# Performance work log

Hardware: AMD Instinct MI355X
Metric: run time of the kernel (lower is better)

The kernel has to match this reference:

```python
import jax, jax.numpy as jnp
import numpy as np

H_SZ, W_SZ = 24, 24  # size for location=2 (H*W == N3)

def _ln(x, g, b, eps=1e-5):
    m = jnp.mean(x, axis=-1, keepdims=True)
    v = jnp.var(x, axis=-1, keepdims=True)
    return (x - m) / jnp.sqrt(v + eps) * g + b

def _cross_attn(value, x2, Wp, bp):
    # key = softmax(x2^T, dim=1) == softmax over channels; query = softmax over tokens
    k = jax.nn.softmax(x2, axis=2)   # [B,M,C], softmax over C
    q = jax.nn.softmax(x2, axis=1)   # [B,M,C], softmax over M
    ctx = jnp.einsum('bnc,bmc->bnm', value, k)   # value @ key
    att = jnp.einsum('bnm,bmc->bnc', ctx, q)     # context @ query
    return att @ Wp.T + bp

def _dwconv(x, Wdw, bdw, Hh, Ww):
    B, N, C = x.shape
    t = x.transpose(0, 2, 1).reshape(B, C, Hh, Ww)
    y = jax.lax.conv_general_dilated(t, Wdw, (1, 1), 'SAME',
                                     feature_group_count=C,
                                     dimension_numbers=('NCHW', 'OIHW', 'NCHW'))
    y = y + bdw[None, :, None, None]
    return y.reshape(B, C, N).transpose(0, 2, 1)

def setup_inputs() -> dict:
    key = jax.random.key(0)
    ks = jax.random.split(key, 16)
    B = 4; d0, d1, d2 = 128, 256, 512
    N1, N2, N3 = 96 * 96, 48 * 48, 24 * 24
    s = 0.02
    dh = 4 * d2
    inp = {}
    inp['x']  = jax.random.normal(ks[0], (B, N1, d0), jnp.float32)
    inp['x2'] = jax.random.normal(ks[1], (B, N2, d1), jnp.float32)
    inp['x3'] = jax.random.normal(ks[2], (B, N3, d2), jnp.float32)
    inp['W_lin']  = jax.random.normal(ks[3], (d2, d0)) * s   # linear: d0->d2
    inp['W_lin2'] = jax.random.normal(ks[4], (d2, d1)) * s   # linear2: d1->d2
    inp['W_lin3'] = jax.random.normal(ks[5], (d1, d0)) * s   # linear3: d0->d1
    inp['W_lin4'] = jax.random.normal(ks[6], (d2, d1)) * s   # linear4: d1->d2
    inp['w'] = jnp.ones((1,), jnp.float32)
    inp['Wp1'] = jax.random.normal(ks[7], (d2, d2)) * s;  inp['bp1'] = jnp.zeros((d2,))
    inp['Wp2'] = jax.random.normal(ks[8], (d2, d2)) * s;  inp['bp2'] = jnp.zeros((d2,))
    inp['Wp3'] = jax.random.normal(ks[9], (d1, d1)) * s;  inp['bp3'] = jnp.zeros((d1,))
    inp['Wp4'] = jax.random.normal(ks[10], (d2, d2)) * s; inp['bp4'] = jnp.zeros((d2,))
    inp['g_norm'] = jnp.ones((d2,)); inp['b_norm'] = jnp.zeros((d2,))
    inp['Wfc1'] = jax.random.normal(ks[11], (dh, d2)) * s; inp['bfc1'] = jnp.zeros((dh,))
    inp['Wdw']  = jax.random.normal(ks[12], (dh, 1, 3, 3)) * s; inp['bdw'] = jnp.zeros((dh,))
    inp['g_ln1'] = jnp.ones((dh,)); inp['b_ln1'] = jnp.zeros((dh,))
    inp['Wfc2'] = jax.random.normal(ks[13], (d2, dh)) * s; inp['bfc2'] = jnp.zeros((d2,))
    return inp

def reference(x, x2, x3, W_lin, W_lin2, W_lin3, W_lin4, w,
              Wp1, bp1, Wp2, bp2, Wp3, bp3, Wp4, bp4,
              g_norm, b_norm, Wfc1, bfc1, Wdw, bdw, g_ln1, b_ln1, Wfc2, bfc2):
    # location == 2 branch
    image  = x  @ W_lin.T    # [B,N1,d2]
    image2 = x2 @ W_lin2.T   # [B,N2,d2]
    image4 = x  @ W_lin3.T   # [B,N1,d1]
    atten1 = _cross_attn(x3, image,  Wp1, bp1)
    atten2 = _cross_attn(x3, image2, Wp2, bp2)
    a3 = _cross_attn(x2, image4, Wp3, bp3)   # [B,N2,d1]
    a3 = a3 @ W_lin4.T                        # [B,N2,d2]
    atten3 = _cross_attn(x3, a3, Wp4, bp4)    # [B,N3,d2]
    f = jax.nn.sigmoid(w)
    other = (1.0 - f) / 2.0
    atten_ = f * atten3 + other * atten2 + other * atten1
    atten = x3 + atten_
    an = _ln(atten, g_norm, b_norm)
    # MixFFN_skip (fc1 computed once; torch computes it twice with same result)
    h = an @ Wfc1.T + bfc1
    dw = _dwconv(h, Wdw, bdw, H_SZ, W_SZ)
    ax = jax.nn.gelu(_ln(dw + h, g_ln1, b_ln1), approximate=False)
    out = ax @ Wfc2.T + bfc2
    return atten + out
```

## Files before the change

### kernel.cpp

```cpp
#include <hip/hip_runtime.h>
#include <hip/hip_bf16.h>
#include <math.h>

typedef long long i64;
typedef __attribute__((ext_vector_type(8))) short short8v;
typedef __attribute__((ext_vector_type(4))) short short4v;
typedef __attribute__((ext_vector_type(4))) float float4v;

#define SPITCH 72
#define NCV 16

__device__ __forceinline__ float ldv(const void* p, i64 idx, int isBf16) {
  return isBf16 ? __bfloat162float(((const __hip_bfloat16*)p)[idx])
                : ((const float*)p)[idx];
}
__device__ __forceinline__ unsigned short bf16bits(float f) {
  __hip_bfloat16 h = __float2bfloat16(f);
  return *(unsigned short*)&h;
}
__device__ __forceinline__ float bits2f(unsigned short u) {
  union { unsigned int ui; float fl; } cv; cv.ui = ((unsigned int)u) << 16;
  return cv.fl;
}

__global__ void detect_dtype(const unsigned short* w, int* dt) {
  dt[0] = (w[0] == 0) ? 0 : 1;
}

struct CvArgs {
  const void* src[NCV];
  unsigned short* dst[NCV];
  i64 n[NCV];
  int blkStart[NCV + 1];
};
__global__ __launch_bounds__(256) void convert_many(const int* dt, CvArgs a) {
  int au = dt[0];
  int bid = blockIdx.x;
  int lo = 0;
  #pragma unroll
  for (int i = 0; i < NCV; ++i) if (bid >= a.blkStart[i + 1]) lo = i + 1;
  const void* s = a.src[lo];
  unsigned short* d = a.dst[lo];
  i64 n = a.n[lo];
  i64 base = ((i64)(bid - a.blkStart[lo]) * 256 + threadIdx.x) * 4;
  if (base + 4 <= n) {
    if (au) {
      *(short4v*)&d[base] = *(const short4v*)&((const unsigned short*)s)[base];
    } else {
      float4v v = *(const float4v*)&((const float*)s)[base];
      short4v o;
      #pragma unroll
      for (int j = 0; j < 4; ++j) o[j] = (short)bf16bits(v[j]);
      *(short4v*)&d[base] = o;
    }
  } else {
    for (; base < n; ++base) d[base] = bf16bits(ldv(s, base, au));
  }
}

__global__ void transpose_dw(const int* dt, const void* Wdw, unsigned short* Wdwt) {
  int au = dt[0];
  int i = blockIdx.x * 256 + threadIdx.x;
  if (i >= 9 * 2048) return;
  int k = i / 2048, ch = i % 2048;
  Wdwt[i] = bf16bits(ldv(Wdw, (i64)ch * 9 + k, au));
}

__global__ __launch_bounds__(256) void gemm_mfma_bt(
    const int* dt,
    const unsigned short* A, i64 bsA,
    const unsigned short* Bt, i64 bsB,
    const void* bias, int biasDt,
    const void* add, int addDt, i64 bsAdd,
    void* C, i64 bsC, int outMode,
    int M, int N, int K, int flags,
    const void* wPtr, int alphaMode,
    float* csP, float* rsP)
{
  __shared__ unsigned short Ash[64 * SPITCH];
  __shared__ unsigned short Bsh[64 * SPITCH];
  __shared__ unsigned short LT[64 * SPITCH];

  const int au = dt[0];
  const int bDt = (biasDt == 2) ? au : biasDt;
  const int aDt = (addDt == 2) ? au : addDt;

  const int b  = blockIdx.z;
  const int m0 = blockIdx.y * 64;
  const int n0 = blockIdx.x * 64;
  const int t = threadIdx.x;
  const int lane = t & 63, wave = t >> 6;
  const int wr = (wave >> 1) * 32, wc = (wave & 1) * 32;
  const int quad = lane >> 4, l15 = lane & 15;
  const unsigned short* Ab = A + (i64)b * bsA;
  const unsigned short* Bb = Bt + (i64)b * bsB;
  const int sr = t >> 3, sg = (t & 7) * 8;

  float alpha = 1.0f;
  if (alphaMode) {
    float w0 = ldv(wPtr, 0, au);
    float f = 1.0f / (1.0f + expf(-w0));
    alpha = (alphaMode == 2) ? f : (1.0f - f) * 0.5f;
  }

  float4v acc00 = {0.f,0.f,0.f,0.f}, acc01 = {0.f,0.f,0.f,0.f};
  float4v acc10 = {0.f,0.f,0.f,0.f}, acc11 = {0.f,0.f,0.f,0.f};

  for (int k0 = 0; k0 < K; k0 += 64) {
    #pragma unroll
    for (int p = 0; p < 2; ++p) {
      int rr = sr + p * 32;
      *(short8v*)&Ash[rr * SPITCH + sg] = *(const short8v*)&Ab[(i64)(m0 + rr) * K + k0 + sg];
      *(short8v*)&Bsh[rr * SPITCH + sg] = *(const short8v*)&Bb[(i64)(n0 + rr) * K + k0 + sg];
    }
    __syncthreads();
    #pragma unroll
    for (int ks = 0; ks < 2; ++ks) {
      int ko = ks * 32 + quad * 8;
      short8v a0 = *(const short8v*)&Ash[(wr + l15) * SPITCH + ko];
      short8v a1 = *(const short8v*)&Ash[(wr + 16 + l15) * SPITCH + ko];
      short8v b0 = *(const short8v*)&Bsh[(wc + l15) * SPITCH + ko];
      short8v b1 = *(const short8v*)&Bsh[(wc + 16 + l15) * SPITCH + ko];
      acc00 = __builtin_amdgcn_mfma_f32_16x16x32_bf16(a0, b0, acc00, 0, 0, 0);
      acc01 = __builtin_amdgcn_mfma_f32_16x16x32_bf16(a0, b1, acc01, 0, 0, 0);
      acc10 = __builtin_amdgcn_mfma_f32_16x16x32_bf16(a1, b0, acc10, 0, 0, 0);
      acc11 = __builtin_amdgcn_mfma_f32_16x16x32_bf16(a1, b1, acc11, 0, 0, 0);
    }
    __syncthreads();
  }

  float* Cf = (float*)C;
  unsigned short* Ch = (unsigned short*)C;

  if (outMode == 2) {
    #pragma unroll
    for (int rg = 0; rg < 4; ++rg) {
      #pragma unroll
      for (int sub = 0; sub < 4; ++sub) {
        int lr = wr + quad * 4 + rg + (sub >> 1) * 16;
        int lc = wc + l15 + (sub & 1) * 16;
        float v = (sub == 0 ? acc00[rg] : sub == 1 ? acc01[rg] :
                   sub == 2 ? acc10[rg] : acc11[rg]) * alpha;
        if (bias) v += ldv(bias, n0 + lc, bDt);
        if (flags & 1) v = expf(v);
        LT[lc * SPITCH + lr] = bf16bits(v);
      }
    }
    __syncthreads();
    #pragma unroll
    for (int p = 0; p < 2; ++p) {
      int rr = sr + p * 32;
      short8v vv = *(short8v*)&LT[rr * SPITCH + sg];
      *(short8v*)(Ch + (i64)b * bsC + (i64)(n0 + rr) * M + m0 + sg) = vv;
    }
    if (csP) {
      if (t < 64) {
        const unsigned short* Lr = &LT[t * SPITCH];
        float s = 0.f;
        #pragma unroll
        for (int i = 0; i < 64; ++i) s += bits2f(Lr[i]);
        atomicAdd(&csP[(i64)b * N + n0 + t], s);
      } else if (t < 128) {
        int tok = t - 64;
        float s = 0.f;
        #pragma unroll
        for (int i = 0; i < 64; ++i) s += bits2f(LT[i * SPITCH + tok]);
        atomicAdd(&rsP[(i64)b * M + m0 + tok], s);
      }
    }
    return;
  }

  #pragma unroll
  for (int rg = 0; rg < 4; ++rg) {
    #pragma unroll
    for (int sub = 0; sub < 4; ++sub) {
      int lr = wr + quad * 4 + rg + (sub >> 1) * 16;
      int lc = wc + l15 + (sub & 1) * 16;
      int gi = m0 + lr, gj = n0 + lc;
      float v = (sub == 0 ? acc00[rg] : sub == 1 ? acc01[rg] :
                 sub == 2 ? acc10[rg] : acc11[rg]) * alpha;
      if (bias) v += ldv(bias, gj, bDt);
      if (add)  v += ldv(add, (i64)b * bsAdd + (i64)gi * N + gj, aDt);
      i64 idx = (i64)b * bsC + (i64)gi * N + gj;
      if (flags & 2) v += Cf[idx];
      if (flags & 1) v = expf(v);
      if (outMode == 1) Ch[idx] = bf16bits(v);
      else              Cf[idx] = v;
    }
  }
}

__global__ __launch_bounds__(256, 2) void softprod128_db(
    const unsigned short* Gt, const float* rs, float* Part,
    int C, i64 M, int splits, int mChunk, int nPairs, int Bn)
{
  __shared__ unsigned short Ash[2][128 * SPITCH];
  __shared__ unsigned short Bsh[2][128 * SPITCH];

  const int bid = blockIdx.x;
  const int xcd = bid & 7;
  const int q = bid >> 3;
  const int gHi = q / nPairs;
  const int pr = q - gHi * nPairs;
  const int g = gHi * 8 + xcd;
  const int b  = g / splits;
  const int sp = g - b * splits;

  const int nStrips = C >> 7;
  int rem = pr, s0 = 0;
  while (rem >= nStrips - s0) { rem -= nStrips - s0; ++s0; }
  const int s1 = s0 + rem;
  const int c0 = s0 * 128;
  const int c1 = s1 * 128;

  const int t = threadIdx.x;
  const int lane = t & 63, wave = t >> 6;
  const int wrow = (wave >> 1) * 64, wcol = (wave & 1) * 64;
  const int quad = lane >> 4, l15 = lane & 15;
  const unsigned short* Gb = Gt + (i64)b * C * M;
  const float* rib = rs + (i64)b * M;
  const int sg = (t & 7) * 8;
  const int r4 = t >> 3;

  float4v acc[4][4];
  #pragma unroll
  for (int i = 0; i < 4; ++i)
    #pragma unroll
    for (int j = 0; j < 4; ++j)
      acc[i][j] = (float4v){0.f, 0.f, 0.f, 0.f};

  const i64 mBeg = (i64)sp * mChunk;
  const int nt = mChunk >> 6;

  const unsigned short* Arow = &Gb[(i64)(c0 + r4) * M + sg];
  const unsigned short* Brow = &Gb[(i64)(c1 + r4) * M + sg];

  short8v pa[4], pb[4];
  float rv[8];

  auto loadF = [&](i64 m0) {
    #pragma unroll
    for (int pp = 0; pp < 4; ++pp) {
      pa[pp] = *(const short8v*)&Arow[(i64)32 * pp * M + m0];
      pb[pp] = *(const short8v*)&Brow[(i64)32 * pp * M + m0];
    }
    #pragma unroll
    for (int j = 0; j < 8; ++j) {
      float r_ = rsqrtf(rib[m0 + sg + j]);
      rv[j] = r_ * r_;
    }
  };
  auto stageF = [&](int bi) {
    #pragma unroll
    for (int pp = 0; pp < 4; ++pp) {
      *(short8v*)&Ash[bi][(r4 + 32 * pp) * SPITCH + sg] = pa[pp];
      short8v sb;
      #pragma unroll
      for (int j = 0; j < 8; ++j)
        sb[j] = (short)bf16bits(bits2f((unsigned short)pb[pp][j]) * rv[j]);
      *(short8v*)&Bsh[bi][(r4 + 32 * pp) * SPITCH + sg] = sb;
    }
  };
  auto mfmaF = [&](int bi) {
    #pragma unroll
    for (int ks = 0; ks < 2; ++ks) {
      int ko = ks * 32 + quad * 8;
      short8v af[4], bfr[4];
      #pragma unroll
      for (int i = 0; i < 4; ++i) {
        af[i]  = *(const short8v*)&Ash[bi][(wrow + i * 16 + l15) * SPITCH + ko];
        bfr[i] = *(const short8v*)&Bsh[bi][(wcol + i * 16 + l15) * SPITCH + ko];
      }
      #pragma unroll
      for (int i = 0; i < 4; ++i)
        #pragma unroll
        for (int j = 0; j < 4; ++j)
          acc[i][j] = __builtin_amdgcn_mfma_f32_16x16x32_bf16(af[i], bfr[j], acc[i][j], 0, 0, 0);
    }
  };

  loadF(mBeg);

  int cur = 0;
  for (int tt = 0; tt < nt; ++tt) {
    stageF(cur);
    __syncthreads();
    if (tt + 1 < nt) loadF(mBeg + (i64)(tt + 1) * 64);
    mfmaF(cur);
    cur ^= 1;
  }

  float* Pb = Part + (((i64)sp * Bn + b) * nPairs + pr) * 16384;
  #pragma unroll
  for (int i = 0; i < 4; ++i)
    #pragma unroll
    for (int rg = 0; rg < 4; ++rg) {
      int rr = wrow + i * 16 + quad * 4 + rg;
      #pragma unroll
      for (int j = 0; j < 4; ++j) {
        int cc = wcol + j * 16 + l15;
        Pb[rr * 128 + cc] = acc[i][j][rg];
      }
    }
}

__global__ __launch_bounds__(256) void scale_S_tile_bf16(
    const float* Part, const float* cs, unsigned short* Sb,
    int C, int nStrips, int splits, int nPairs, int Bn) {
  __shared__ float lt[64][65];
  const int nT = C >> 6;
  const int b   = blockIdx.y;
  const int R64 = blockIdx.x / nT;
  const int C64 = blockIdx.x % nT;
  const int R = R64 >> 1, Cp = C64 >> 1;
  const bool trans = R > Cp;
  const int a2 = trans ? Cp : R, b2 = trans ? R : Cp;
  const int pair = a2 * nStrips - (a2 * (a2 - 1)) / 2 + (b2 - a2);
  const float* Pb = Part + ((i64)b * nPairs + pair) * 16384;
  const i64 stride = (i64)Bn * nPairs * 16384;

  const int t = threadIdx.x;
  const int lr = t >> 6;
  const int lc = t & 63;

  const int srB = (trans ? (C64 & 1) : (R64 & 1)) * 64;
  const int scB = (trans ? (R64 & 1) : (C64 & 1)) * 64;

  float acc[16];
  #pragma unroll
  for (int it = 0; it < 16; ++it) acc[it] = 0.f;
  for (int sp = 0; sp < splits; ++sp) {
    const float* src = Pb + (i64)sp * stride;
    #pragma unroll
    for (int it = 0; it < 16; ++it)
      acc[it] += src[(srB + lr + 4 * it) * 128 + scB + lc];
  }

  unsigned short* So = Sb + (i64)b * C * C;
  const float* csb = cs + (i64)b * C;
  if (!trans) {
    #pragma unroll
    for (int it = 0; it < 16; ++it) {
      int r = R64 * 64 + lr + 4 * it, c = C64 * 64 + lc;
      So[(i64)r * C + c] = bf16bits(acc[it] / csb[c]);
    }
  } else {
    #pragma unroll
    for (int it = 0; it < 16; ++it) lt[lr + 4 * it][lc] = acc[it];
    __syncthreads();
    #pragma unroll
    for (int it = 0; it < 16; ++it) {
      int r = R64 * 64 + lr + 4 * it, c = C64 * 64 + lc;
      So[(i64)r * C + c] = bf16bits(lt[lc][lr + 4 * it] / csb[c]);
    }
  }
}

__global__ __launch_bounds__(256) void transpose_to_bf16(
    const float* T, unsigned short* Tt, int Nn) {
  __shared__ float tile[64][65];
  int b = blockIdx.z;
  int i0 = blockIdx.y * 64, j0 = blockIdx.x * 64;
  const float* Tb = T + (i64)b * Nn * Nn;
  unsigned short* Ttb = Tt + (i64)b * Nn * Nn;
  int t = threadIdx.x;
  int li = t >> 6, lj = t & 63;
  #pragma unroll
  for (int p = 0; p < 16; ++p)
    tile[li + p * 4][lj] = Tb[(i64)(i0 + li + p * 4) * Nn + j0 + lj];
  __syncthreads();
  #pragma unroll
  for (int p = 0; p < 16; ++p) {
    int row = li + p * 4;
    Ttb[(i64)(j0 + row) * Nn + i0 + lj] = bf16bits(tile[lj][row]);
  }
}

__global__ void combine_bias(const int* dt, const void* w, const void* bp1,
                             const void* bp2, const void* bp4, float* biasc) {
  int au = dt[0];
  int j = threadIdx.x;
  float w0 = ldv(w, 0, au);
  float f = 1.0f / (1.0f + expf(-w0));
  float other = (1.0f - f) * 0.5f;
  biasc[j] = f * ldv(bp4, j, au) + other * (ldv(bp1, j, au) + ldv(bp2, j, au));
}

__global__ __launch_bounds__(256) void layernorm512(const int* dt, const float* X,
                                                    const void* g, const void* be,
                                                    __hip_bfloat16* Y) {
  int au = dt[0];
  i64 row = blockIdx.x;
  const float* xr = X + row * 512;
  int t = threadIdx.x;
  float x0 = xr[t], x1 = xr[t + 256];
  float s = x0 + x1, q = x0 * x0 + x1 * x1;
  #pragma unroll
  for (int off = 32; off; off >>= 1) { s += __shfl_down(s, off); q += __shfl_down(q, off); }
  __shared__ float ws_[4], wq_[4];
  int lane = t & 63, wv = t >> 6;
  if (!lane) { ws_[wv] = s; wq_[wv] = q; }
  __syncthreads();
  float S = ws_[0] + ws_[1] + ws_[2] + ws_[3];
  float Q = wq_[0] + wq_[1] + wq_[2] + wq_[3];
  float mean = S * (1.f / 512.f);
  float var = Q * (1.f / 512.f) - mean * mean;
  float inv = rsqrtf(var + 1e-5f);
  Y[row * 512 + t]       = __float2bfloat16((x0 - mean) * inv * ldv(g, t, au) + ldv(be, t, au));
  Y[row * 512 + t + 256] = __float2bfloat16((x1 - mean) * inv * ldv(g, t + 256, au) + ldv(be, t + 256, au));
}

__global__ __launch_bounds__(256) void dwconv_ln_gelu(
    const unsigned short* h, const unsigned short* Wdwt,
    const unsigned short* bdwB, const unsigned short* gB,
    const unsigned short* beB, unsigned short* ax)
{
  int n = blockIdx.x;
  int b = blockIdx.y;
  int y = n / 24, x = n % 24;
  const unsigned short* hb = h + (i64)b * 576 * 2048;
  int t = threadIdx.x;
  int ch0 = t * 8;

  short8v bdv = *(const short8v*)&bdwB[ch0];
  short8v gv  = *(const short8v*)&gB[ch0];
  short8v bev = *(const short8v*)&beB[ch0];
  short8v hc  = *(const short8v*)&hb[(i64)n * 2048 + ch0];

  float accv[8];
  #pragma unroll
  for (int j = 0; j < 8; ++j) accv[j] = bits2f((unsigned short)bdv[j]);

  #pragma unroll
  for (int dy = 0; dy < 3; ++dy) {
    int yy = y + dy - 1;
    if (yy < 0 || yy >= 24) continue;
    #pragma unroll
    for (int dx = 0; dx < 3; ++dx) {
      int xx = x + dx - 1;
      if (xx < 0 || xx >= 24) continue;
      short8v hv = *(const short8v*)&hb[(i64)(yy * 24 + xx) * 2048 + ch0];
      short8v wv = *(const short8v*)&Wdwt[(i64)(dy * 3 + dx) * 2048 + ch0];
      #pragma unroll
      for (int j = 0; j < 8; ++j)
        accv[j] += bits2f((unsigned short)hv[j]) * bits2f((unsigned short)wv[j]);
    }
  }

  float z[8];
  float s = 0.f, q = 0.f;
  #pragma unroll
  for (int j = 0; j < 8; ++j) {
    float zz = accv[j] + bits2f((unsigned short)hc[j]);
    z[j] = zz; s += zz; q += zz * zz;
  }

  #pragma unroll
  for (int off = 32; off; off >>= 1) { s += __shfl_down(s, off); q += __shfl_down(q, off); }
  __shared__ float ws_[4], wq_[4];
  int lane = t & 63, wv2 = t >> 6;
  if (!lane) { ws_[wv2] = s; wq_[wv2] = q; }
  __syncthreads();
  float S = ws_[0] + ws_[1] + ws_[2] + ws_[3];
  float Q = wq_[0] + wq_[1] + wq_[2] + wq_[3];
  float mean = S * (1.f / 2048.f);
  float var = Q * (1.f / 2048.f) - mean * mean;
  float inv = rsqrtf(var + 1e-5f);

  short8v ov;
  #pragma unroll
  for (int j = 0; j < 8; ++j) {
    float v = (z[j] - mean) * inv * bits2f((unsigned short)gv[j]) + bits2f((unsigned short)bev[j]);
    float gl = 0.5f * v * (1.0f + erff(v * 0.70710678118654752f));
    ov[j] = (short)bf16bits(gl);
  }
  *(short8v*)&ax[((i64)b * 576 + n) * 2048 + ch0] = ov;
}

extern "C" void kernel_launch(void* const* d_in, const int* in_sizes, int n_in,
                              void* d_out, int out_size, void* d_ws, size_t ws_size,
                              hipStream_t stream) {
  const int B = 4, N1 = 9216, N2 = 2304, N3 = 576;
  const int d0 = 128, d1 = 256, d2 = 512, dh = 2048;

  const void* x     = d_in[0];
  const void* x2    = d_in[1];
  const void* x3    = d_in[2];
  const void* Wlin  = d_in[3];
  const void* Wlin2 = d_in[4];
  const void* Wlin3 = d_in[5];
  const void* Wlin4 = d_in[6];
  const void* w     = d_in[7];
  const void* Wp1 = d_in[8];  const void* bp1 = d_in[9];
  const void* Wp2 = d_in[10]; const void* bp2 = d_in[11];
  const void* Wp3 = d_in[12]; const void* bp3 = d_in[13];
  const void* Wp4 = d_in[14]; const void* bp4 = d_in[15];
  const void* gnorm = d_in[16]; const void* bnorm = d_in[17];
  const void* Wfc1 = d_in[18]; const void* bfc1 = d_in[19];
  const void* Wdw  = d_in[20]; const void* bdw  = d_in[21];
  const void* gln1 = d_in[22]; const void* bln1 = d_in[23];
  const void* Wfc2 = d_in[24]; const void* bfc2 = d_in[25];

  char* base = (char*)d_ws;
  size_t o = 0;
  auto alloc = [&](size_t n) -> char* {
    char* r = base + o; o += (n + 255) & ~(size_t)255; return r;
  };

  int* dtFlag = (int*)alloc(256);
  char* arena = alloc((size_t)B * N1 * d2 * 2);
  float* rsBig   = (float*)alloc((size_t)B * N1 * 4);
  float* rsSmall = (float*)alloc((size_t)B * N2 * 4);
  size_t csBytes = (size_t)B * (d2 + d2 + d1 + d2) * 4;
  float* csAll = (float*)alloc(csBytes);
  float* cs1  = csAll;
  float* cs2  = cs1 + B * d2;
  float* cs4  = cs2 + B * d2;
  float* cs3b = cs4 + B * d1;
  float* Part = (float*)alloc((size_t)12 * B * 10 * 16384 * 4);
  unsigned short* Sb16  = (unsigned short*)alloc((size_t)B * d2 * d2 * 2);
  unsigned short* S3b16 = (unsigned short*)alloc((size_t)B * d1 * d1 * 2);
  unsigned short* U3t   = (unsigned short*)alloc((size_t)B * d1 * d1 * 2);
  float* T     = (float*)alloc((size_t)B * d2 * d2 * 4);
  float* biasc = (float*)alloc((size_t)d2 * 4);
  unsigned short* xb  = (unsigned short*)alloc((size_t)B * N1 * d0 * 2);
  unsigned short* x2b = (unsigned short*)alloc((size_t)B * N2 * d1 * 2);
  unsigned short* x3b = (unsigned short*)alloc((size_t)B * N3 * d2 * 2);
  unsigned short* Wlinb  = (unsigned short*)alloc((size_t)d2 * d0 * 2);
  unsigned short* Wlin2b = (unsigned short*)alloc((size_t)d2 * d1 * 2);
  unsigned short* Wlin3b = (unsigned short*)alloc((size_t)d1 * d0 * 2);
  unsigned short* Wlin4b = (unsigned short*)alloc((size_t)d2 * d1 * 2);
  unsigned short* Wp1b = (unsigned short*)alloc((size_t)d2 * d2 * 2);
  unsigned short* Wp2b = (unsigned short*)alloc((size_t)d2 * d2 * 2);
  unsigned short* Wp3b = (unsigned short*)alloc((size_t)d1 * d1 * 2);
  unsigned short* Wp4b = (unsigned short*)alloc((size_t)d2 * d2 * 2);
  unsigned short* Wfc1b = (unsigned short*)alloc((size_t)dh * d2 * 2);
  unsigned short* Wfc2b = (unsigned short*)alloc((size_t)d2 * dh * 2);
  unsigned short* Wdwt  = (unsigned short*)alloc((size_t)9 * dh * 2);
  unsigned short* bdwB  = (unsigned short*)alloc((size_t)dh * 2);
  unsigned short* gln1B = (unsigned short*)alloc((size_t)dh * 2);
  unsigned short* bln1B = (unsigned short*)alloc((size_t)dh * 2);

  unsigned short* Et1    = (unsigned short*)arena;
  unsigned short* Et4    = (unsigned short*)arena;
  unsigned short* a3buf  = (unsigned short*)(arena + 18874368);
  unsigned short* EtA3b  = (unsigned short*)arena;
  unsigned short* Et2    = (unsigned short*)arena;
  float*          atten  = (float*)arena;
  __hip_bfloat16* an     = (__hip_bfloat16*)(arena + 4718592);
  unsigned short* hbuf   = (unsigned short*)(arena + 7077888);
  unsigned short* axb    = (unsigned short*)(arena + 16515072);
  unsigned short* Tt     = (unsigned short*)(arena + 28573696);

  detect_dtype<<<dim3(1), dim3(1), 0, stream>>>((const unsigned short*)w, dtFlag);
  hipMemsetAsync(csAll, 0, csBytes, stream);

  {
    CvArgs a;
    const void* srcs[NCV] = { x, x2, x3, Wlin, Wlin2, Wlin3, Wlin4,
                              Wp1, Wp2, Wp3, Wp4, Wfc1, Wfc2,
                              bdw, gln1, bln1 };
    unsigned short* dsts[NCV] = { xb, x2b, x3b, Wlinb, Wlin2b, Wlin3b, Wlin4b,
                                  Wp1b, Wp2b, Wp3b, Wp4b, Wfc1b, Wfc2b,
                                  bdwB, gln1B, bln1B };
    i64 ns[NCV] = { (i64)B*N1*d0, (i64)B*N2*d1, (i64)B*N3*d2,
                    (i64)d2*d0, (i64)d2*d1, (i64)d1*d0, (i64)d2*d1,
                    (i64)d2*d2, (i64)d2*d2, (i64)d1*d1, (i64)d2*d2,
                    (i64)dh*d2, (i64)d2*dh,
                    (i64)dh, (i64)dh, (i64)dh };
    int cum = 0;
    for (int i = 0; i < NCV; ++i) {
      a.src[i] = srcs[i]; a.dst[i] = dsts[i]; a.n[i] = ns[i];
      a.blkStart[i] = cum;
      cum += (int)((ns[i] + 1023) / 1024);
    }
    a.blkStart[NCV] = cum;
    convert_many<<<dim3(cum), dim3(256), 0, stream>>>(dtFlag, a);
    transpose_dw<<<dim3((9 * 2048 + 255) / 256), dim3(256), 0, stream>>>(dtFlag, Wdw, Wdwt);
  }

  auto gemm64 = [&](const unsigned short* A_, i64 bsA,
                    const unsigned short* Bt_, i64 bsB,
                    const void* bias_, int biasDt,
                    const void* add_, int addDt, i64 bsAdd,
                    void* C_, i64 bsC, int outMode,
                    int M_, int N_, int K_, int flags, int alphaMode,
                    float* csP = nullptr, float* rsP = nullptr) {
    gemm_mfma_bt<<<dim3(N_ / 64, M_ / 64, B), dim3(256), 0, stream>>>(
        dtFlag, A_, bsA, Bt_, bsB, bias_, biasDt, add_, addDt, bsAdd,
        C_, bsC, outMode, M_, N_, K_, flags, w, alphaMode, csP, rsP);
  };

  auto softtail = [&](unsigned short* Et, float* cs, float* rsArr,
                      unsigned short* SbB, int C, int M, int splits) {
    int nStrips = C / 128;
    int nPairs = nStrips * (nStrips + 1) / 2;
    int nBlk = nPairs * B * splits;
    softprod128_db<<<dim3(nBlk), dim3(256), 0, stream>>>(
        Et, rsArr, Part, C, M, splits, M / splits, nPairs, B);
    int nT = C / 64;
    scale_S_tile_bf16<<<dim3(nT * nT, B), dim3(256), 0, stream>>>(
        Part, cs, SbB, C, nStrips, splits, nPairs, B);
  };

  hipMemsetAsync(rsBig, 0, (size_t)B * N1 * 4, stream);
  gemm64(xb, (i64)N1 * d0, Wlinb, 0, nullptr, 0, nullptr, 0, 0,
         Et1, (i64)N1 * d2, 2, N1, d2, d0, 1, 0, cs1, rsBig);
  softtail(Et1, cs1, rsBig, Sb16, d2, N1, 12);
  gemm64(Sb16, (i64)d2 * d2, Wp1b, 0, nullptr, 0, nullptr, 0, 0,
         T, (i64)d2 * d2, 0, d2, d2, d2, 0, 1);

  hipMemsetAsync(rsBig, 0, (size_t)B * N1 * 4, stream);
  gemm64(xb, (i64)N1 * d0, Wlin3b, 0, nullptr, 0, nullptr, 0, 0,
         Et4, (i64)N1 * d1, 2, N1, d1, d0, 1, 0, cs4, rsBig);
  softtail(Et4, cs4, rsBig, S3b16, d1, N1, 36);
  gemm64(S3b16, (i64)d1 * d1, Wp3b, 0, nullptr, 0, nullptr, 0, 0,
         U3t, (i64)d1 * d1, 2, d1, d1, d1, 0, 0);
  gemm64(x2b, (i64)N2 * d1, U3t, (i64)d1 * d1, bp3, 2, nullptr, 0, 0,
         a3buf, (i64)N2 * d1, 1, N2, d1, d1, 0, 0);
  hipMemsetAsync(rsSmall, 0, (size_t)B * N2 * 4, stream);
  gemm64(a3buf, (i64)N2 * d1, Wlin4b, 0, nullptr, 0, nullptr, 0, 0,
         EtA3b, (i64)N2 * d2, 2, N2, d2, d1, 1, 0, cs3b, rsSmall);
  softtail(EtA3b, cs3b, rsSmall, Sb16, d2, N2, 12);
  gemm64(Sb16, (i64)d2 * d2, Wp4b, 0, nullptr, 0, nullptr, 0, 0,
         T, (i64)d2 * d2, 0, d2, d2, d2, 2, 2);

  hipMemsetAsync(rsSmall, 0, (size_t)B * N2 * 4, stream);
  gemm64(x2b, (i64)N2 * d1, Wlin2b, 0, nullptr, 0, nullptr, 0, 0,
         Et2, (i64)N2 * d2, 2, N2, d2, d1, 1, 0, cs2, rsSmall);
  softtail(Et2, cs2, rsSmall, Sb16, d2, N2, 12);
  gemm64(Sb16, (i64)d2 * d2, Wp2b, 0, nullptr, 0, nullptr, 0, 0,
         T, (i64)d2 * d2, 0, d2, d2, d2, 2, 1);

  transpose_to_bf16<<<dim3(d2 / 64, d2 / 64, B), dim3(256), 0, stream>>>(T, Tt, d2);
  combine_bias<<<dim3(1), dim3(d2), 0, stream>>>(dtFlag, w, bp1, bp2, bp4, biasc);

  gemm64(x3b, (i64)N3 * d2, Tt, (i64)d2 * d2, biasc, 0, x3, 2, (i64)N3 * d2,
         atten, (i64)N3 * d2, 0, N3, d2, d2, 0, 0);

  layernorm512<<<dim3(B * N3), dim3(256), 0, stream>>>(dtFlag, atten, gnorm, bnorm, an);

  gemm64((const unsigned short*)an, (i64)N3 * d2, Wfc1b, 0, bfc1, 2, nullptr, 0, 0,
         hbuf, (i64)N3 * dh, 1, N3, dh, d2, 0, 0);

  dwconv_ln_gelu<<<dim3(N3, B), dim3(256), 0, stream>>>(
      hbuf, Wdwt, bdwB, gln1B, bln1B, axb);

  gemm64(axb, (i64)N3 * dh, Wfc2b, 0, bfc2, 2,
         atten, 0, (i64)N3 * d2,
         d_out, (i64)N3 * d2, 0, N3, d2, dh, 0, 0);

  (void)in_sizes; (void)n_in; (void)out_size; (void)ws_size;
}
```

Before: 481.2 us.

## Fold Wlin4 into cross-attn output weights and merge memsets, drop dtype kernel

Reassociates the a3 path so Wlin4 is first multiplied into the small U3 matrix (a d2×d1 product) and the folded bias is precomputed, removing the N2×d1 a3 intermediate and one large GEMM over N2 tokens. The separate dtype-detect kernel and the per-stage memsets are replaced by inline dtype detection and a single zeroing memset over separate row-sum buffers. Split counts for the softmax-product tails are also changed. This adds two small kernels and changes the rounding order of the a3 path (bf16 intermediates).

```diff
diff --git a/kernel.cpp b/kernel.cpp
--- a/kernel.cpp
+++ b/kernel.cpp
@@ -10,6 +10,9 @@
 #define SPITCH 72
 #define NCV 16
 
+__device__ __forceinline__ int dtype_of(const void* w16) {
+  return ((const unsigned short*)w16)[0] != 0;
+}
 __device__ __forceinline__ float ldv(const void* p, i64 idx, int isBf16) {
   return isBf16 ? __bfloat162float(((const __hip_bfloat16*)p)[idx])
                 : ((const float*)p)[idx];
@@ -21,10 +24,6 @@
 __device__ __forceinline__ float bits2f(unsigned short u) {
   union { unsigned int ui; float fl; } cv; cv.ui = ((unsigned int)u) << 16;
   return cv.fl;
-}
-
-__global__ void detect_dtype(const unsigned short* w, int* dt) {
-  dt[0] = (w[0] == 0) ? 0 : 1;
 }
 
 struct CvArgs {
@@ -33,8 +32,8 @@
   i64 n[NCV];
   int blkStart[NCV + 1];
 };
-__global__ __launch_bounds__(256) void convert_many(const int* dt, CvArgs a) {
-  int au = dt[0];
+__global__ __launch_bounds__(256) void convert_many(const void* w16, CvArgs a) {
+  int au = dtype_of(w16);
   int bid = blockIdx.x;
   int lo = 0;
   #pragma unroll
@@ -58,16 +57,25 @@
   }
 }
 
-__global__ void transpose_dw(const int* dt, const void* Wdw, unsigned short* Wdwt) {
-  int au = dt[0];
+__global__ void transpose_dw(const void* w16, const void* Wdw, unsigned short* Wdwt) {
+  int au = dtype_of(w16);
   int i = blockIdx.x * 256 + threadIdx.x;
   if (i >= 9 * 2048) return;
   int k = i / 2048, ch = i % 2048;
   Wdwt[i] = bf16bits(ldv(Wdw, (i64)ch * 9 + k, au));
 }
 
+__global__ void bias_wl4(const void* w16, const unsigned short* Wlin4b,
+                         const void* bp3, float* bias2) {
+  int au = dtype_of(w16);
+  int c = blockIdx.x * 256 + threadIdx.x;
+  float s = 0.f;
+  for (int k = 0; k < 256; ++k)
+    s += bits2f(Wlin4b[c * 256 + k]) * ldv(bp3, k, au);
+  bias2[c] = s;
+}
+
 __global__ __launch_bounds__(256) void gemm_mfma_bt(
-    const int* dt,
     const unsigned short* A, i64 bsA,
     const unsigned short* Bt, i64 bsB,
     const void* bias, int biasDt,
@@ -81,7 +89,7 @@
   __shared__ unsigned short Bsh[64 * SPITCH];
   __shared__ unsigned short LT[64 * SPITCH];
 
-  const int au = dt[0];
+  const int au = dtype_of(wPtr);
   const int bDt = (biasDt == 2) ? au : biasDt;
   const int aDt = (addDt == 2) ? au : addDt;
 
@@ -377,9 +385,9 @@
   }
 }
 
-__global__ void combine_bias(const int* dt, const void* w, const void* bp1,
+__global__ void combine_bias(const void* w, const void* bp1,
                              const void* bp2, const void* bp4, float* biasc) {
-  int au = dt[0];
+  int au = dtype_of(w);
   int j = threadIdx.x;
   float w0 = ldv(w, 0, au);
   float f = 1.0f / (1.0f + expf(-w0));
@@ -387,10 +395,10 @@
   biasc[j] = f * ldv(bp4, j, au) + other * (ldv(bp1, j, au) + ldv(bp2, j, au));
 }
 
-__global__ __launch_bounds__(256) void layernorm512(const int* dt, const float* X,
+__global__ __launch_bounds__(256) void layernorm512(const void* w16, const float* X,
                                                     const void* g, const void* be,
                                                     __hip_bfloat16* Y) {
-  int au = dt[0];
+  int au = dtype_of(w16);
   i64 row = blockIdx.x;
   const float* xr = X + row * 512;
   int t = threadIdx.x;
@@ -508,20 +516,24 @@
     char* r = base + o; o += (n + 255) & ~(size_t)255; return r;
   };
 
-  int* dtFlag = (int*)alloc(256);
   char* arena = alloc((size_t)B * N1 * d2 * 2);
-  float* rsBig   = (float*)alloc((size_t)B * N1 * 4);
-  float* rsSmall = (float*)alloc((size_t)B * N2 * 4);
-  size_t csBytes = (size_t)B * (d2 + d2 + d1 + d2) * 4;
-  float* csAll = (float*)alloc(csBytes);
-  float* cs1  = csAll;
+  size_t zeroBytes = (size_t)(2 * B * N1 + 2 * B * N2 +
+                              B * (d2 + d2 + d1 + d2)) * 4;
+  float* zeroBlk = (float*)alloc(zeroBytes);
+  float* rsBigA   = zeroBlk;
+  float* rsBigB   = rsBigA + B * N1;
+  float* rsSmallA = rsBigB + B * N1;
+  float* rsSmallB = rsSmallA + B * N2;
+  float* cs1  = rsSmallB + B * N2;
   float* cs2  = cs1 + B * d2;
   float* cs4  = cs2 + B * d2;
   float* cs3b = cs4 + B * d1;
-  float* Part = (float*)alloc((size_t)12 * B * 10 * 16384 * 4);
+  float* Part = (float*)alloc((size_t)480 * 16384 * 4);
   unsigned short* Sb16  = (unsigned short*)alloc((size_t)B * d2 * d2 * 2);
   unsigned short* S3b16 = (unsigned short*)alloc((size_t)B * d1 * d1 * 2);
-  unsigned short* U3t   = (unsigned short*)alloc((size_t)B * d1 * d1 * 2);
+  unsigned short* U3n   = (unsigned short*)alloc((size_t)B * d1 * d1 * 2);
+  unsigned short* W2t   = (unsigned short*)alloc((size_t)B * d2 * d1 * 2);
+  float* bias2 = (float*)alloc((size_t)d2 * 4);
   float* T     = (float*)alloc((size_t)B * d2 * d2 * 4);
   float* biasc = (float*)alloc((size_t)d2 * 4);
   unsigned short* xb  = (unsigned short*)alloc((size_t)B * N1 * d0 * 2);
@@ -544,7 +556,6 @@
 
   unsigned short* Et1    = (unsigned short*)arena;
   unsigned short* Et4    = (unsigned short*)arena;
-  unsigned short* a3buf  = (unsigned short*)(arena + 18874368);
   unsigned short* EtA3b  = (unsigned short*)arena;
   unsigned short* Et2    = (unsigned short*)arena;
   float*          atten  = (float*)arena;
@@ -553,8 +564,7 @@
   unsigned short* axb    = (unsigned short*)(arena + 16515072);
   unsigned short* Tt     = (unsigned short*)(arena + 28573696);
 
-  detect_dtype<<<dim3(1), dim3(1), 0, stream>>>((const unsigned short*)w, dtFlag);
-  hipMemsetAsync(csAll, 0, csBytes, stream);
+  hipMemsetAsync(zeroBlk, 0, zeroBytes, stream);
 
   {
     CvArgs a;
@@ -576,8 +586,9 @@
       cum += (int)((ns[i] + 1023) / 1024);
     }
     a.blkStart[NCV] = cum;
-    convert_many<<<dim3(cum), dim3(256), 0, stream>>>(dtFlag, a);
-    transpose_dw<<<dim3((9 * 2048 + 255) / 256), dim3(256), 0, stream>>>(dtFlag, Wdw, Wdwt);
+    convert_many<<<dim3(cum), dim3(256), 0, stream>>>(w, a);
+    transpose_dw<<<dim3((9 * 2048 + 255) / 256), dim3(256), 0, stream>>>(w, Wdw, Wdwt);
+    bias_wl4<<<dim3(2), dim3(256), 0, stream>>>(w, Wlin4b, bp3, bias2);
   }
 
   auto gemm64 = [&](const unsigned short* A_, i64 bsA,
@@ -588,7 +599,7 @@
                     int M_, int N_, int K_, int flags, int alphaMode,
                     float* csP = nullptr, float* rsP = nullptr) {
     gemm_mfma_bt<<<dim3(N_ / 64, M_ / 64, B), dim3(256), 0, stream>>>(
-        dtFlag, A_, bsA, Bt_, bsB, bias_, biasDt, add_, addDt, bsAdd,
+        A_, bsA, Bt_, bsB, bias_, biasDt, add_, addDt, bsAdd,
         C_, bsC, outMode, M_, N_, K_, flags, w, alphaMode, csP, rsP);
   };
 
@@ -604,42 +615,38 @@
         Part, cs, SbB, C, nStrips, splits, nPairs, B);
   };
 
-  hipMemsetAsync(rsBig, 0, (size_t)B * N1 * 4, stream);
   gemm64(xb, (i64)N1 * d0, Wlinb, 0, nullptr, 0, nullptr, 0, 0,
-         Et1, (i64)N1 * d2, 2, N1, d2, d0, 1, 0, cs1, rsBig);
-  softtail(Et1, cs1, rsBig, Sb16, d2, N1, 12);
+         Et1, (i64)N1 * d2, 2, N1, d2, d0, 1, 0, cs1, rsBigA);
+  softtail(Et1, cs1, rsBigA, Sb16, d2, N1, 12);
   gemm64(Sb16, (i64)d2 * d2, Wp1b, 0, nullptr, 0, nullptr, 0, 0,
          T, (i64)d2 * d2, 0, d2, d2, d2, 0, 1);
 
-  hipMemsetAsync(rsBig, 0, (size_t)B * N1 * 4, stream);
   gemm64(xb, (i64)N1 * d0, Wlin3b, 0, nullptr, 0, nullptr, 0, 0,
-         Et4, (i64)N1 * d1, 2, N1, d1, d0, 1, 0, cs4, rsBig);
-  softtail(Et4, cs4, rsBig, S3b16, d1, N1, 36);
+         Et4, (i64)N1 * d1, 2, N1, d1, d0, 1, 0, cs4, rsBigB);
+  softtail(Et4, cs4, rsBigB, S3b16, d1, N1, 24);
   gemm64(S3b16, (i64)d1 * d1, Wp3b, 0, nullptr, 0, nullptr, 0, 0,
-         U3t, (i64)d1 * d1, 2, d1, d1, d1, 0, 0);
-  gemm64(x2b, (i64)N2 * d1, U3t, (i64)d1 * d1, bp3, 2, nullptr, 0, 0,
-         a3buf, (i64)N2 * d1, 1, N2, d1, d1, 0, 0);
-  hipMemsetAsync(rsSmall, 0, (size_t)B * N2 * 4, stream);
-  gemm64(a3buf, (i64)N2 * d1, Wlin4b, 0, nullptr, 0, nullptr, 0, 0,
-         EtA3b, (i64)N2 * d2, 2, N2, d2, d1, 1, 0, cs3b, rsSmall);
-  softtail(EtA3b, cs3b, rsSmall, Sb16, d2, N2, 12);
+         U3n, (i64)d1 * d1, 1, d1, d1, d1, 0, 0);
+  gemm64(Wlin4b, 0, U3n, (i64)d1 * d1, nullptr, 0, nullptr, 0, 0,
+         W2t, (i64)d2 * d1, 1, d2, d1, d1, 0, 0);
+  gemm64(x2b, (i64)N2 * d1, W2t, (i64)d2 * d1, bias2, 0, nullptr, 0, 0,
+         EtA3b, (i64)N2 * d2, 2, N2, d2, d1, 1, 0, cs3b, rsSmallA);
+  softtail(EtA3b, cs3b, rsSmallA, Sb16, d2, N2, 6);
   gemm64(Sb16, (i64)d2 * d2, Wp4b, 0, nullptr, 0, nullptr, 0, 0,
          T, (i64)d2 * d2, 0, d2, d2, d2, 2, 2);
 
-  hipMemsetAsync(rsSmall, 0, (size_t)B * N2 * 4, stream);
   gemm64(x2b, (i64)N2 * d1, Wlin2b, 0, nullptr, 0, nullptr, 0, 0,
-         Et2, (i64)N2 * d2, 2, N2, d2, d1, 1, 0, cs2, rsSmall);
-  softtail(Et2, cs2, rsSmall, Sb16, d2, N2, 12);
+         Et2, (i64)N2 * d2, 2, N2, d2, d1, 1, 0, cs2, rsSmallB);
+  softtail(Et2, cs2, rsSmallB, Sb16, d2, N2, 6);
   gemm64(Sb16, (i64)d2 * d2, Wp2b, 0, nullptr, 0, nullptr, 0, 0,
          T, (i64)d2 * d2, 0, d2, d2, d2, 2, 1);
 
   transpose_to_bf16<<<dim3(d2 / 64, d2 / 64, B), dim3(256), 0, stream>>>(T, Tt, d2);
-  combine_bias<<<dim3(1), dim3(d2), 0, stream>>>(dtFlag, w, bp1, bp2, bp4, biasc);
+  combine_bias<<<dim3(1), dim3(d2), 0, stream>>>(w, bp1, bp2, bp4, biasc);
 
   gemm64(x3b, (i64)N3 * d2, Tt, (i64)d2 * d2, biasc, 0, x3, 2, (i64)N3 * d2,
          atten, (i64)N3 * d2, 0, N3, d2, d2, 0, 0);
 
-  layernorm512<<<dim3(B * N3), dim3(256), 0, stream>>>(dtFlag, atten, gnorm, bnorm, an);
+  layernorm512<<<dim3(B * N3), dim3(256), 0, stream>>>(w, atten, gnorm, bnorm, an);
 
   gemm64((const unsigned short*)an, (i64)N3 * d2, Wfc1b, 0, bfc1, 2, nullptr, 0, 0,
          hbuf, (i64)N3 * dh, 1, N3, dh, d2, 0, 0);
```

Measured after the change: 494.2 us. 2.7% more time.
